# Performance work log

Measured on AMD Instinct MI355X. Metric: run time of the kernel, lower is better.

## Reference

```python
import jax, jax.numpy as jnp
import numpy as np

RNN = 1024     # rnn_size
POSE = 135     # config.pose_size (15 joints x 3x3 rotmat)
SEED = 120     # seed_seq_len
TGT = 24       # target_seq_len
B = 256        # batch size


def setup_inputs() -> dict:
    key = jax.random.key(0)
    k0, k1, k2, k3, k4 = jax.random.split(key, 5)
    s = 1.0 / np.sqrt(RNN)
    poses = jax.random.normal(k0, (B, SEED + TGT, POSE), dtype=jnp.float32)
    # nn.LSTMCell(input_size, rnn_size, bias=False): weights U(-1/sqrt(H), 1/sqrt(H))
    W_ih = jax.random.uniform(k1, (4 * RNN, POSE), minval=-s, maxval=s, dtype=jnp.float32)
    W_hh = jax.random.uniform(k2, (4 * RNN, RNN), minval=-s, maxval=s, dtype=jnp.float32)
    # nn.Linear(rnn_size, pose_size)
    W_fc = jax.random.uniform(k3, (POSE, RNN), minval=-s, maxval=s, dtype=jnp.float32)
    b_fc = jax.random.uniform(k4, (POSE,), minval=-s, maxval=s, dtype=jnp.float32)
    return {"poses": poses, "W_ih": W_ih, "W_hh": W_hh, "W_fc": W_fc, "b_fc": b_fc}


def reference(poses, W_ih, W_hh, W_fc, b_fc):
    def cell(x, h, c):
        # PyTorch LSTMCell gate order: i, f, g, o ; bias=False
        gates = x @ W_ih.T + h @ W_hh.T          # [B, 4*RNN]
        i, f, g, o = jnp.split(gates, 4, axis=-1)
        c_new = jax.nn.sigmoid(f) * c + jax.nn.sigmoid(i) * jnp.tanh(g)
        h_new = jax.nn.sigmoid(o) * jnp.tanh(c_new)
        return h_new, c_new

    # Encoder: steps over poses[:, 0:SEED-1] (dropout p=0 -> identity)
    enc_inputs = jnp.transpose(poses[:, : SEED - 1], (1, 0, 2))  # [SEED-1, B, POSE]
    h0 = jnp.zeros((B, RNN), dtype=poses.dtype)
    c0 = jnp.zeros((B, RNN), dtype=poses.dtype)

    def enc_step(carry, x):
        h, c = carry
        h, c = cell(x, h, c)
        return (h, c), None

    (h, c), _ = jax.lax.scan(enc_step, (h0, c0), enc_inputs)

    # first decoder input (poses[:, SEED-1]) is ground truth. inp is detached.
    inp0 = poses[:, SEED - 1]  # [B, POSE]

    def dec_step(carry, _):
        h, c, inp = carry
        inp = jax.lax.stop_gradient(inp)  # inp.detach() in the original
        h, c = cell(inp, h, c)
        out = inp + h @ W_fc.T + b_fc     # residual + linear decode
        return (h, c, out), out

    _, outs = jax.lax.scan(dec_step, (h, c, inp0), None, length=TGT)  # [TGT, B, POSE]
    return jnp.transpose(outs, (1, 0, 2))  # predictions [B, TGT, POSE]
```

## Files before the change

kernel.cpp:

```cpp
#include <hip/hip_runtime.h>
#include <stdint.h>

#define NB 256
#define NH 1024
#define NPOSE 135
#define NPPAD 160
#define NSTEPS 143
#define NDEC 24
#define KTOT 1184
#define LSTR 168
#define NWG 256

typedef __bf16 bf16;
typedef __attribute__((ext_vector_type(8))) __bf16 bf16x8;
typedef __attribute__((ext_vector_type(4))) float f32x4;
typedef __attribute__((ext_vector_type(4))) uint32_t u32x4;

#define WCAT_OFF 0
#define WCAT_BYTES (4096l * KTOT * 2)
#define WFC_OFF  (WCAT_OFF + WCAT_BYTES)
#define WFC_BYTES (144l * 1024 * 2)
#define X_OFF    (WFC_OFF + WFC_BYTES)
#define X_BYTES  (143l * NB * NPPAD * 2)
#define H_OFF    (X_OFF + X_BYTES)
#define H_BYTES  (2l * NB * NH * 2)
#define BAR_OFF  (H_OFF + H_BYTES)
#define BAR_BYTES 16384

__device__ __forceinline__ u32x4 llc_ld16(const void* p) {
  u32x4 v;
  asm volatile("global_load_dwordx4 %0, %1, off sc0 sc1"
               : "=v"(v) : "v"(p) : "memory");
  return v;
}
__device__ __forceinline__ u32x4 g_ld16(const void* p) {
  u32x4 v;
  asm volatile("global_load_dwordx4 %0, %1, off"
               : "=v"(v) : "v"(p) : "memory");
  return v;
}
__device__ __forceinline__ void llc_st2(void* p, uint32_t v) {
  asm volatile("global_store_short %0, %1, off sc0 sc1"
               :: "v"(p), "v"(v) : "memory");
}
#define WAIT_VM(n) do { \
    asm volatile("s_waitcnt vmcnt(" #n ")" ::: "memory"); \
    __builtin_amdgcn_sched_barrier(0); } while (0)

#define POLL(ptr, tgt) do { \
    while (__hip_atomic_load((ptr), __ATOMIC_RELAXED, __HIP_MEMORY_SCOPE_AGENT) < (tgt)) \
      __builtin_amdgcn_s_sleep(1); \
  } while (0)

__global__ void k_zero(uint32_t* p, int n) {
  int i = blockIdx.x * blockDim.x + threadIdx.x;
  int st = gridDim.x * blockDim.x;
  for (; i < n; i += st) p[i] = 0u;
}

__global__ void k_wcat(const float* __restrict__ Whh, const float* __restrict__ Wih,
                       bf16* __restrict__ W) {
  int n = blockIdx.x;
  for (int kk = threadIdx.x; kk < KTOT; kk += blockDim.x) {
    float v = 0.f;
    if (kk < NH) v = Whh[(size_t)n * NH + kk];
    else if (kk - NH < NPOSE) v = Wih[(size_t)n * NPOSE + (kk - NH)];
    W[(size_t)n * KTOT + kk] = (bf16)v;
  }
}

__global__ void k_wfc(const float* __restrict__ Wfc, bf16* __restrict__ W) {
  int p = blockIdx.x;
  for (int kk = threadIdx.x; kk < NH; kk += blockDim.x) {
    float v = (p < NPOSE) ? Wfc[(size_t)p * NH + kk] : 0.f;
    W[(size_t)p * NH + kk] = (bf16)v;
  }
}

__global__ void k_x(const float* __restrict__ poses, bf16* __restrict__ X) {
  int idx = blockIdx.x;
  int t = idx >> 8, b = idx & 255;
  int p = threadIdx.x;
  if (p < NPPAD) {
    float v = (p < NPOSE) ? poses[((size_t)b * 144 + t) * NPOSE + p] : 0.f;
    X[(size_t)idx * NPPAD + p] = (bf16)v;
  }
}

__device__ __forceinline__ float sigm(float x) { return 1.f / (1.f + __expf(-x)); }
__device__ __forceinline__ float tanh_(float x) {
  float e = __expf(2.f * x);
  return 1.f - 2.f / (e + 1.f);
}

__global__ __launch_bounds__(256, 1) void
k_main(const float* __restrict__ poses, const float* __restrict__ bfc,
       const bf16* __restrict__ Wcat, const bf16* __restrict__ Wfcb,
       bf16* __restrict__ X, bf16* __restrict__ H, int* __restrict__ bar,
       float* __restrict__ out) {
  __shared__ bf16 BldsH[8 * 64 * 128];
  __shared__ bf16 BldsX[64 * LSTR];

  const int tid  = threadIdx.x;
  const int lane = tid & 63;
  const int wv   = tid >> 6;
  const int cl   = lane & 15;
  const int quad = lane >> 4;
  const int L    = blockIdx.x;
  const int jb = (L & 7) * 8 + ((L >> 3) & 7);
  const int bb = L >> 6;
  const int b0 = bb * 64;
  const int j0 = jb * 16;
  const int mych = jb >> 3;
  const bool is_out = ((L & 7) == 7) && (((L >> 3) & 7) < 4);
  const int brow0 = bb * 64 + ((L >> 3) & 7) * 16;

  for (int t = tid; t < 8 * 64 * 16; t += 256) {
    int c = t >> 10, rem = t & 1023, r = rem >> 4, xb = rem & 15;
    u32x4 v = *(const u32x4*)&Wcat[(size_t)((r >> 4) * NH + j0 + (r & 15)) * KTOT
                                   + c * 128 + xb * 8];
    *(u32x4*)&BldsH[(c * 64 + r) * 128 + ((xb ^ (r & 15)) << 3)] = v;
  }
  for (int it = 0; it < 5; ++it) {
    int u = tid + it * 256, r = u / 20, iu = u % 20;
    u32x4 v = *(const u32x4*)&Wcat[(size_t)((r >> 4) * NH + j0 + (r & 15)) * KTOT
                                   + 1024 + iu * 8];
    *(u32x4*)&BldsX[r * LSTR + iu * 8] = v;
  }
  __syncthreads();

  const int arow = b0 + wv * 16 + cl;
  const size_t aBase  = (size_t)arow * NH + quad * 8;
  const size_t axBase = (size_t)arow * NPPAD + quad * 8;

  u32x4 A0[4], A1[4], A2[4], AX[5];
  f32x4 acc[4];
  float cst[4] = {0.f, 0.f, 0.f, 0.f};

#define ISSUE_AH(SET, HP, chn) do { \
    const bf16* ga_ = (HP) + aBase + (chn) * 128; \
    SET[0] = llc_ld16(ga_);      SET[1] = llc_ld16(ga_ + 32); \
    SET[2] = llc_ld16(ga_ + 64); SET[3] = llc_ld16(ga_ + 96); } while (0)
#define ISSUE_AX(sv) do { \
    const bf16* ga_ = X + (size_t)(sv) * NB * NPPAD + axBase; \
    if ((sv) < 120) { \
      AX[0] = g_ld16(ga_);        AX[1] = g_ld16(ga_ + 32); \
      AX[2] = g_ld16(ga_ + 64);   AX[3] = g_ld16(ga_ + 96); \
      AX[4] = g_ld16(ga_ + 128); \
    } else { \
      AX[0] = llc_ld16(ga_);      AX[1] = llc_ld16(ga_ + 32); \
      AX[2] = llc_ld16(ga_ + 64); AX[3] = llc_ld16(ga_ + 96); \
      AX[4] = llc_ld16(ga_ + 128); \
    } } while (0)
#define MFMA_LDS(SET, c) do { \
    _Pragma("unroll") \
    for (int ks = 0; ks < 4; ++ks) { \
      bf16x8 af_ = __builtin_bit_cast(bf16x8, SET[ks]); \
      _Pragma("unroll") \
      for (int gb = 0; gb < 4; ++gb) { \
        bf16x8 bw_ = *(const bf16x8*)&BldsH[((c) * 64 + gb * 16 + cl) * 128 \
                                            + (((ks * 4 + quad) ^ cl) << 3)]; \
        acc[gb] = __builtin_amdgcn_mfma_f32_16x16x32_bf16(af_, bw_, acc[gb], 0, 0, 0); \
      } } } while (0)
#define MFMA_X() do { \
    _Pragma("unroll") \
    for (int ks = 0; ks < 5; ++ks) { \
      bf16x8 af_ = __builtin_bit_cast(bf16x8, AX[ks]); \
      _Pragma("unroll") \
      for (int gb = 0; gb < 4; ++gb) { \
        bf16x8 bw_ = *(const bf16x8*)&BldsX[(gb * 16 + cl) * LSTR + ks * 32 + quad * 8]; \
        acc[gb] = __builtin_amdgcn_mfma_f32_16x16x32_bf16(af_, bw_, acc[gb], 0, 0, 0); \
      } } } while (0)
#define POLL_ALL8(tgt) do { \
    for (;;) { int ok_ = 1; \
      _Pragma("unroll") \
      for (int c_ = 0; c_ < 8; ++c_) \
        ok_ &= (__hip_atomic_load(&bar[(bb * 8 + c_) * 32], __ATOMIC_RELAXED, \
                                  __HIP_MEMORY_SCOPE_AGENT) >= (tgt)); \
      if (ok_) break; __builtin_amdgcn_s_sleep(1); } } while (0)

  ISSUE_AH(A0, H, 0);
  ISSUE_AH(A1, H, 1);

  for (int s = 0; s < NSTEPS; ++s) {
    const bf16* Hr = H + (size_t)(s & 1) * (NB * NH);
    bf16* Hw = H + (size_t)((s + 1) & 1) * (NB * NH);
    #pragma unroll
    for (int gb = 0; gb < 4; ++gb) acc[gb] = f32x4{0, 0, 0, 0};

    ISSUE_AH(A2, Hr, 2); WAIT_VM(8); MFMA_LDS(A0, 0);
    ISSUE_AH(A0, Hr, 3); WAIT_VM(8); MFMA_LDS(A1, 1);
    ISSUE_AH(A1, Hr, 4); WAIT_VM(8); MFMA_LDS(A2, 2);
    ISSUE_AH(A2, Hr, 5); WAIT_VM(8); MFMA_LDS(A0, 3);
    ISSUE_AH(A0, Hr, 6); WAIT_VM(8); MFMA_LDS(A1, 4);
    ISSUE_AH(A1, Hr, 7); WAIT_VM(8); MFMA_LDS(A2, 5);
    if (s >= 120) POLL(&bar[(32 + bb) * 32], 4 * (s - 119));
    ISSUE_AX(s);         WAIT_VM(9); MFMA_LDS(A0, 6);
                         WAIT_VM(5); MFMA_LDS(A1, 7);
                         WAIT_VM(0); MFMA_X();

    #pragma unroll
    for (int r = 0; r < 4; ++r) {
      float gi = sigm(acc[0][r]);
      float gf = sigm(acc[1][r]);
      float gg = tanh_(acc[2][r]);
      float go = sigm(acc[3][r]);
      float cn = gf * cst[r] + gi * gg;
      cst[r] = cn;
      float h = go * tanh_(cn);
      bf16 hb = (bf16)h;
      llc_st2(&Hw[(size_t)(b0 + wv * 16 + quad * 4 + r) * NH + j0 + cl],
              (uint32_t)__builtin_bit_cast(uint16_t, hb));
    }
    WAIT_VM(0);
    __syncthreads();
    if (tid == 0) atomicAdd(&bar[(bb * 8 + mych) * 32], 1);

    if (s >= 119 && is_out) {
      const int k = s - 119;
      POLL_ALL8(8 * (s + 1));
      f32x4 oa[3] = {{0,0,0,0},{0,0,0,0},{0,0,0,0}};
      const bf16* hrow = Hw + (size_t)(brow0 + cl) * NH;
      for (int kb = 0; kb < 4; ++kb) {
        u32x4 hv[8];
        #pragma unroll
        for (int t = 0; t < 8; ++t)
          hv[t] = llc_ld16(&hrow[(kb * 8 + t) * 32 + quad * 8]);
        WAIT_VM(0);
        #pragma unroll
        for (int t = 0; t < 8; ++t) {
          bf16x8 af = __builtin_bit_cast(bf16x8, hv[t]);
          #pragma unroll
          for (int i = 0; i < 3; ++i) {
            int ct = wv + i * 4;
            if (ct > 8) continue;
            bf16x8 bw = *(const bf16x8*)&Wfcb[(size_t)(ct * 16 + cl) * NH
                                              + (kb * 8 + t) * 32 + quad * 8];
            oa[i] = __builtin_amdgcn_mfma_f32_16x16x32_bf16(af, bw, oa[i], 0, 0, 0);
          }
        }
      }
      #pragma unroll
      for (int i = 0; i < 3; ++i) {
        int ct = wv + i * 4;
        if (ct > 8) continue;
        int p = ct * 16 + cl;
        if (p < NPOSE) {
          #pragma unroll
          for (int r = 0; r < 4; ++r) {
            int b = brow0 + quad * 4 + r;
            float inp = (k == 0) ? poses[((size_t)b * 144 + 119) * NPOSE + p]
                                 : out[((size_t)b * NDEC + (k - 1)) * NPOSE + p];
            float v = oa[i][r] + inp + bfc[p];
            out[((size_t)b * NDEC + k) * NPOSE + p] = v;
            if (s + 1 < NSTEPS) {
              bf16 xb = (bf16)v;
              llc_st2(&X[((size_t)(s + 1) * NB + b) * NPPAD + p],
                      (uint32_t)__builtin_bit_cast(uint16_t, xb));
            }
          }
        }
      }
      if (s + 1 < NSTEPS) {
        WAIT_VM(0);
        __syncthreads();
        if (tid == 0) atomicAdd(&bar[(32 + bb) * 32], 1);
      }
    }

    if (s + 1 < NSTEPS) {
      POLL_ALL8(8 * (s + 1));
      ISSUE_AH(A0, Hw, 0);
      ISSUE_AH(A1, Hw, 1);
    }
  }
}

extern "C" void kernel_launch(void* const* d_in, const int* in_sizes, int n_in,
                              void* d_out, int out_size, void* d_ws, size_t ws_size,
                              hipStream_t stream) {
  const float* poses = (const float*)d_in[0];
  const float* Wih   = (const float*)d_in[1];
  const float* Whh   = (const float*)d_in[2];
  const float* Wfc   = (const float*)d_in[3];
  const float* bfc   = (const float*)d_in[4];
  if (ws_size < (size_t)(BAR_OFF + BAR_BYTES)) return;

  char* ws = (char*)d_ws;
  bf16* Wcat = (bf16*)(ws + WCAT_OFF);
  bf16* Wfcb = (bf16*)(ws + WFC_OFF);
  bf16* X    = (bf16*)(ws + X_OFF);
  bf16* H    = (bf16*)(ws + H_OFF);
  int*  bar  = (int*)(ws + BAR_OFF);

  k_zero<<<256, 256, 0, stream>>>((uint32_t*)(ws + H_OFF), (int)((H_BYTES + BAR_BYTES) / 4));
  k_zero<<<256, 256, 0, stream>>>((uint32_t*)(X + (size_t)120 * NB * NPPAD),
                                  (int)(23l * NB * NPPAD * 2 / 4));
  k_wcat<<<4096, 256, 0, stream>>>(Whh, Wih, Wcat);
  k_wfc<<<144, 256, 0, stream>>>(Wfc, Wfcb);
  k_x<<<120 * 256, 256, 0, stream>>>(poses, X);
  k_main<<<NWG, 256, 0, stream>>>(poses, bfc, Wcat, Wfcb, X, H, bar, (float*)d_out);
}
```

Measured before the change: 1.644 ms.

## Switch recurrent GEMM to 32x32x16 MFMA with two-wave workgroups

Each workgroup now runs 2 waves instead of 4, each wave owning 32 batch rows and issuing 32x32x16 bf16 MFMAs into two 16-float accumulators. The four gates are regrouped with cross-lane shuffles before the cell update. Three H chunks are prefetched ahead instead of two, and the 8-counter barrier poll becomes one lane-parallel load reduced with __all. The aim is fewer MFMA and LDS read instructions per step and cheaper polling, at the cost of more registers per wave and fewer waves to hide latency.

```diff
diff --git a/kernel.cpp b/kernel.cpp
--- a/kernel.cpp
+++ b/kernel.cpp
@@ -14,6 +14,7 @@
 typedef __bf16 bf16;
 typedef __attribute__((ext_vector_type(8))) __bf16 bf16x8;
 typedef __attribute__((ext_vector_type(4))) float f32x4;
+typedef __attribute__((ext_vector_type(16))) float f32x16;
 typedef __attribute__((ext_vector_type(4))) uint32_t u32x4;
 
 #define WCAT_OFF 0
@@ -51,6 +52,13 @@
     while (__hip_atomic_load((ptr), __ATOMIC_RELAXED, __HIP_MEMORY_SCOPE_AGENT) < (tgt)) \
       __builtin_amdgcn_s_sleep(1); \
   } while (0)
+#define POLL_ALL8(tgt) do { \
+    for (;;) { \
+      int v_ = __hip_atomic_load(&bar[(bb * 8 + (lane & 7)) * 32], \
+                                 __ATOMIC_RELAXED, __HIP_MEMORY_SCOPE_AGENT); \
+      if (__all(v_ >= (tgt))) break; \
+      __builtin_amdgcn_s_sleep(1); \
+    } } while (0)
 
 __global__ void k_zero(uint32_t* p, int n) {
   int i = blockIdx.x * blockDim.x + threadIdx.x;
@@ -93,7 +101,7 @@
   return 1.f - 2.f / (e + 1.f);
 }
 
-__global__ __launch_bounds__(256, 1) void
+__global__ __launch_bounds__(128, 1) void
 k_main(const float* __restrict__ poses, const float* __restrict__ bfc,
        const bf16* __restrict__ Wcat, const bf16* __restrict__ Wfcb,
        bf16* __restrict__ X, bf16* __restrict__ H, int* __restrict__ bar,
@@ -104,6 +112,9 @@
   const int tid  = threadIdx.x;
   const int lane = tid & 63;
   const int wv   = tid >> 6;
+  const int lrow = lane & 31;
+  const int half = lane >> 5;
+  const int l15  = lane & 15;
   const int cl   = lane & 15;
   const int quad = lane >> 4;
   const int L    = blockIdx.x;
@@ -115,101 +126,102 @@
   const bool is_out = ((L & 7) == 7) && (((L >> 3) & 7) < 4);
   const int brow0 = bb * 64 + ((L >> 3) & 7) * 16;
 
-  for (int t = tid; t < 8 * 64 * 16; t += 256) {
+  for (int t = tid; t < 8 * 64 * 16; t += 128) {
     int c = t >> 10, rem = t & 1023, r = rem >> 4, xb = rem & 15;
     u32x4 v = *(const u32x4*)&Wcat[(size_t)((r >> 4) * NH + j0 + (r & 15)) * KTOT
                                    + c * 128 + xb * 8];
     *(u32x4*)&BldsH[(c * 64 + r) * 128 + ((xb ^ (r & 15)) << 3)] = v;
   }
-  for (int it = 0; it < 5; ++it) {
-    int u = tid + it * 256, r = u / 20, iu = u % 20;
+  for (int t = tid; t < 64 * 20; t += 128) {
+    int r = t / 20, iu = t % 20;
     u32x4 v = *(const u32x4*)&Wcat[(size_t)((r >> 4) * NH + j0 + (r & 15)) * KTOT
                                    + 1024 + iu * 8];
     *(u32x4*)&BldsX[r * LSTR + iu * 8] = v;
   }
   __syncthreads();
 
-  const int arow = b0 + wv * 16 + cl;
-  const size_t aBase  = (size_t)arow * NH + quad * 8;
-  const size_t axBase = (size_t)arow * NPPAD + quad * 8;
-
-  u32x4 A0[4], A1[4], A2[4], AX[5];
-  f32x4 acc[4];
-  float cst[4] = {0.f, 0.f, 0.f, 0.f};
+  const int arow = b0 + 32 * wv + lrow;
+  const size_t aBase  = (size_t)arow * NH + half * 8;
+  const size_t axBase = (size_t)arow * NPPAD + half * 8;
+
+  u32x4 A0[8], A1[8], A2[8], AX[10];
+  f32x16 acc0, acc1;
+  float cst[8];
+  #pragma unroll
+  for (int r = 0; r < 8; ++r) cst[r] = 0.f;
 
 #define ISSUE_AH(SET, HP, chn) do { \
     const bf16* ga_ = (HP) + aBase + (chn) * 128; \
-    SET[0] = llc_ld16(ga_);      SET[1] = llc_ld16(ga_ + 32); \
-    SET[2] = llc_ld16(ga_ + 64); SET[3] = llc_ld16(ga_ + 96); } while (0)
+    _Pragma("unroll") \
+    for (int kk_ = 0; kk_ < 8; ++kk_) SET[kk_] = llc_ld16(ga_ + kk_ * 16); } while (0)
 #define ISSUE_AX(sv) do { \
     const bf16* ga_ = X + (size_t)(sv) * NB * NPPAD + axBase; \
     if ((sv) < 120) { \
-      AX[0] = g_ld16(ga_);        AX[1] = g_ld16(ga_ + 32); \
-      AX[2] = g_ld16(ga_ + 64);   AX[3] = g_ld16(ga_ + 96); \
-      AX[4] = g_ld16(ga_ + 128); \
+      _Pragma("unroll") \
+      for (int kk_ = 0; kk_ < 10; ++kk_) AX[kk_] = g_ld16(ga_ + kk_ * 16); \
     } else { \
-      AX[0] = llc_ld16(ga_);      AX[1] = llc_ld16(ga_ + 32); \
-      AX[2] = llc_ld16(ga_ + 64); AX[3] = llc_ld16(ga_ + 96); \
-      AX[4] = llc_ld16(ga_ + 128); \
+      _Pragma("unroll") \
+      for (int kk_ = 0; kk_ < 10; ++kk_) AX[kk_] = llc_ld16(ga_ + kk_ * 16); \
     } } while (0)
-#define MFMA_LDS(SET, c) do { \
+#define MFMA_H(SET, c) do { \
     _Pragma("unroll") \
-    for (int ks = 0; ks < 4; ++ks) { \
-      bf16x8 af_ = __builtin_bit_cast(bf16x8, SET[ks]); \
-      _Pragma("unroll") \
-      for (int gb = 0; gb < 4; ++gb) { \
-        bf16x8 bw_ = *(const bf16x8*)&BldsH[((c) * 64 + gb * 16 + cl) * 128 \
-                                            + (((ks * 4 + quad) ^ cl) << 3)]; \
-        acc[gb] = __builtin_amdgcn_mfma_f32_16x16x32_bf16(af_, bw_, acc[gb], 0, 0, 0); \
-      } } } while (0)
+    for (int kk_ = 0; kk_ < 8; ++kk_) { \
+      bf16x8 af_ = __builtin_bit_cast(bf16x8, SET[kk_]); \
+      int slot_ = ((kk_ * 2 + half) ^ l15) << 3; \
+      bf16x8 b0_ = *(const bf16x8*)&BldsH[((c) * 64 + lrow) * 128 + slot_]; \
+      bf16x8 b1_ = *(const bf16x8*)&BldsH[((c) * 64 + 32 + lrow) * 128 + slot_]; \
+      acc0 = __builtin_amdgcn_mfma_f32_32x32x16_bf16(af_, b0_, acc0, 0, 0, 0); \
+      acc1 = __builtin_amdgcn_mfma_f32_32x32x16_bf16(af_, b1_, acc1, 0, 0, 0); \
+    } } while (0)
 #define MFMA_X() do { \
     _Pragma("unroll") \
-    for (int ks = 0; ks < 5; ++ks) { \
-      bf16x8 af_ = __builtin_bit_cast(bf16x8, AX[ks]); \
-      _Pragma("unroll") \
-      for (int gb = 0; gb < 4; ++gb) { \
-        bf16x8 bw_ = *(const bf16x8*)&BldsX[(gb * 16 + cl) * LSTR + ks * 32 + quad * 8]; \
-        acc[gb] = __builtin_amdgcn_mfma_f32_16x16x32_bf16(af_, bw_, acc[gb], 0, 0, 0); \
-      } } } while (0)
-#define POLL_ALL8(tgt) do { \
-    for (;;) { int ok_ = 1; \
-      _Pragma("unroll") \
-      for (int c_ = 0; c_ < 8; ++c_) \
-        ok_ &= (__hip_atomic_load(&bar[(bb * 8 + c_) * 32], __ATOMIC_RELAXED, \
-                                  __HIP_MEMORY_SCOPE_AGENT) >= (tgt)); \
-      if (ok_) break; __builtin_amdgcn_s_sleep(1); } } while (0)
+    for (int kk_ = 0; kk_ < 10; ++kk_) { \
+      bf16x8 af_ = __builtin_bit_cast(bf16x8, AX[kk_]); \
+      bf16x8 b0_ = *(const bf16x8*)&BldsX[lrow * LSTR + kk_ * 16 + half * 8]; \
+      bf16x8 b1_ = *(const bf16x8*)&BldsX[(32 + lrow) * LSTR + kk_ * 16 + half * 8]; \
+      acc0 = __builtin_amdgcn_mfma_f32_32x32x16_bf16(af_, b0_, acc0, 0, 0, 0); \
+      acc1 = __builtin_amdgcn_mfma_f32_32x32x16_bf16(af_, b1_, acc1, 0, 0, 0); \
+    } } while (0)
 
   ISSUE_AH(A0, H, 0);
   ISSUE_AH(A1, H, 1);
+  ISSUE_AH(A2, H, 2);
 
   for (int s = 0; s < NSTEPS; ++s) {
     const bf16* Hr = H + (size_t)(s & 1) * (NB * NH);
     bf16* Hw = H + (size_t)((s + 1) & 1) * (NB * NH);
+    acc0 = (f32x16)(0.f); acc1 = (f32x16)(0.f);
+
+    WAIT_VM(16); MFMA_H(A0, 0); ISSUE_AH(A0, Hr, 3);
+    WAIT_VM(16); MFMA_H(A1, 1); ISSUE_AH(A1, Hr, 4);
+    WAIT_VM(16); MFMA_H(A2, 2); ISSUE_AH(A2, Hr, 5);
+    WAIT_VM(16); MFMA_H(A0, 3); ISSUE_AH(A0, Hr, 6);
+    WAIT_VM(16); MFMA_H(A1, 4); ISSUE_AH(A1, Hr, 7);
+    WAIT_VM(16); MFMA_H(A2, 5);
+    if (s >= 120) POLL(&bar[(32 + bb) * 32], 4 * (s - 119));
+    ISSUE_AX(s);
+    WAIT_VM(18); MFMA_H(A0, 6);
+    WAIT_VM(10); MFMA_H(A1, 7);
+    WAIT_VM(0);  MFMA_X();
+
     #pragma unroll
-    for (int gb = 0; gb < 4; ++gb) acc[gb] = f32x4{0, 0, 0, 0};
-
-    ISSUE_AH(A2, Hr, 2); WAIT_VM(8); MFMA_LDS(A0, 0);
-    ISSUE_AH(A0, Hr, 3); WAIT_VM(8); MFMA_LDS(A1, 1);
-    ISSUE_AH(A1, Hr, 4); WAIT_VM(8); MFMA_LDS(A2, 2);
-    ISSUE_AH(A2, Hr, 5); WAIT_VM(8); MFMA_LDS(A0, 3);
-    ISSUE_AH(A0, Hr, 6); WAIT_VM(8); MFMA_LDS(A1, 4);
-    ISSUE_AH(A1, Hr, 7); WAIT_VM(8); MFMA_LDS(A2, 5);
-    if (s >= 120) POLL(&bar[(32 + bb) * 32], 4 * (s - 119));
-    ISSUE_AX(s);         WAIT_VM(9); MFMA_LDS(A0, 6);
-                         WAIT_VM(5); MFMA_LDS(A1, 7);
-                         WAIT_VM(0); MFMA_X();
-
-    #pragma unroll
-    for (int r = 0; r < 4; ++r) {
-      float gi = sigm(acc[0][r]);
-      float gf = sigm(acc[1][r]);
-      float gg = tanh_(acc[2][r]);
-      float go = sigm(acc[3][r]);
-      float cn = gf * cst[r] + gi * gg;
-      cst[r] = cn;
-      float h = go * tanh_(cn);
+    for (int r8 = 0; r8 < 8; ++r8) {
+      float s0a = __shfl_xor(acc0[r8], 16);
+      float s0b = __shfl_xor(acc0[r8 + 8], 16);
+      float s1a = __shfl_xor(acc1[r8], 16);
+      float s1b = __shfl_xor(acc1[r8 + 8], 16);
+      const bool lo = (lrow < 16);
+      float iv = lo ? acc0[r8]     : s0b;
+      float fv = lo ? s0a          : acc0[r8 + 8];
+      float gv = lo ? acc1[r8]     : s1b;
+      float ov = lo ? s1a          : acc1[r8 + 8];
+      int reg  = lo ? r8 : (r8 + 8);
+      float cn = sigm(fv) * cst[r8] + sigm(iv) * tanh_(gv);
+      cst[r8] = cn;
+      float h = sigm(ov) * tanh_(cn);
+      int row32 = (reg & 3) + 8 * (reg >> 2) + 4 * half;
       bf16 hb = (bf16)h;
-      llc_st2(&Hw[(size_t)(b0 + wv * 16 + quad * 4 + r) * NH + j0 + cl],
+      llc_st2(&Hw[(size_t)(b0 + 32 * wv + row32) * NH + j0 + l15],
               (uint32_t)__builtin_bit_cast(uint16_t, hb));
     }
     WAIT_VM(0);
@@ -219,7 +231,7 @@
     if (s >= 119 && is_out) {
       const int k = s - 119;
       POLL_ALL8(8 * (s + 1));
-      f32x4 oa[3] = {{0,0,0,0},{0,0,0,0},{0,0,0,0}};
+      f32x4 oa[5] = {{0,0,0,0},{0,0,0,0},{0,0,0,0},{0,0,0,0},{0,0,0,0}};
       const bf16* hrow = Hw + (size_t)(brow0 + cl) * NH;
       for (int kb = 0; kb < 4; ++kb) {
         u32x4 hv[8];
@@ -231,8 +243,8 @@
         for (int t = 0; t < 8; ++t) {
           bf16x8 af = __builtin_bit_cast(bf16x8, hv[t]);
           #pragma unroll
-          for (int i = 0; i < 3; ++i) {
-            int ct = wv + i * 4;
+          for (int i = 0; i < 5; ++i) {
+            int ct = wv + i * 2;
             if (ct > 8) continue;
             bf16x8 bw = *(const bf16x8*)&Wfcb[(size_t)(ct * 16 + cl) * NH
                                               + (kb * 8 + t) * 32 + quad * 8];
@@ -241,8 +253,8 @@
         }
       }
       #pragma unroll
-      for (int i = 0; i < 3; ++i) {
-        int ct = wv + i * 4;
+      for (int i = 0; i < 5; ++i) {
+        int ct = wv + i * 2;
         if (ct > 8) continue;
         int p = ct * 16 + cl;
         if (p < NPOSE) {
@@ -272,6 +284,7 @@
       POLL_ALL8(8 * (s + 1));
       ISSUE_AH(A0, Hw, 0);
       ISSUE_AH(A1, Hw, 1);
+      ISSUE_AH(A2, Hw, 2);
     }
   }
 }
@@ -299,5 +312,5 @@
   k_wcat<<<4096, 256, 0, stream>>>(Whh, Wih, Wcat);
   k_wfc<<<144, 256, 0, stream>>>(Wfc, Wfcb);
   k_x<<<120 * 256, 256, 0, stream>>>(poses, X);
-  k_main<<<NWG, 256, 0, stream>>>(poses, bfc, Wcat, Wfcb, X, H, bar, (float*)d_out);
-}
+  k_main<<<NWG, 128, 0, stream>>>(poses, bfc, Wcat, Wfcb, X, H, bar, (float*)d_out);
+}
```

New measurement: 2.426 ms. +47.6%, slower.

## Give every LSTM step its own hidden-state buffer so reads can use cached loads

Applied to the files above, without the earlier changes.

When the workspace is large enough, the hidden state gets a separate buffer per timestep (144 slices) instead of a double buffer. Each address is then written only once, so H and the decoder-step X reads can switch from cache-bypassing sc0/sc1 loads to ordinary cached loads without the risk of reading stale data. The barrier poll across the eight column groups also becomes one load per lane with a wave-wide vote instead of eight sequential loads. The cost is a much larger workspace footprint, and correctness now depends on no stale lines existing for freshly written addresses.

```diff
diff --git a/kernel.cpp b/kernel.cpp
--- a/kernel.cpp
+++ b/kernel.cpp
@@ -23,8 +23,8 @@
 #define X_OFF    (WFC_OFF + WFC_BYTES)
 #define X_BYTES  (143l * NB * NPPAD * 2)
 #define H_OFF    (X_OFF + X_BYTES)
-#define H_BYTES  (2l * NB * NH * 2)
-#define BAR_OFF  (H_OFF + H_BYTES)
+#define H_BYTES2    (2l * NB * NH * 2)
+#define H_BYTES144  (144l * NB * NH * 2)
 #define BAR_BYTES 16384
 
 __device__ __forceinline__ u32x4 llc_ld16(const void* p) {
@@ -39,6 +39,9 @@
                : "=v"(v) : "v"(p) : "memory");
   return v;
 }
+__device__ __forceinline__ u32x4 ld16sel(const void* p, bool cached) {
+  return cached ? g_ld16(p) : llc_ld16(p);
+}
 __device__ __forceinline__ void llc_st2(void* p, uint32_t v) {
   asm volatile("global_store_short %0, %1, off sc0 sc1"
                :: "v"(p), "v"(v) : "memory");
@@ -51,6 +54,13 @@
     while (__hip_atomic_load((ptr), __ATOMIC_RELAXED, __HIP_MEMORY_SCOPE_AGENT) < (tgt)) \
       __builtin_amdgcn_s_sleep(1); \
   } while (0)
+#define POLL_ALL8(tgt) do { \
+    for (;;) { \
+      int v_ = __hip_atomic_load(&bar[(bb * 8 + (lane & 7)) * 32], \
+                                 __ATOMIC_RELAXED, __HIP_MEMORY_SCOPE_AGENT); \
+      if (__all(v_ >= (tgt))) break; \
+      __builtin_amdgcn_s_sleep(1); \
+    } } while (0)
 
 __global__ void k_zero(uint32_t* p, int n) {
   int i = blockIdx.x * blockDim.x + threadIdx.x;
@@ -93,6 +103,7 @@
   return 1.f - 2.f / (e + 1.f);
 }
 
+template <bool DEEP>
 __global__ __launch_bounds__(256, 1) void
 k_main(const float* __restrict__ poses, const float* __restrict__ bfc,
        const bf16* __restrict__ Wcat, const bf16* __restrict__ Wfcb,
@@ -139,8 +150,8 @@
 
 #define ISSUE_AH(SET, HP, chn) do { \
     const bf16* ga_ = (HP) + aBase + (chn) * 128; \
-    SET[0] = llc_ld16(ga_);      SET[1] = llc_ld16(ga_ + 32); \
-    SET[2] = llc_ld16(ga_ + 64); SET[3] = llc_ld16(ga_ + 96); } while (0)
+    SET[0] = ld16sel(ga_, DEEP);      SET[1] = ld16sel(ga_ + 32, DEEP); \
+    SET[2] = ld16sel(ga_ + 64, DEEP); SET[3] = ld16sel(ga_ + 96, DEEP); } while (0)
 #define ISSUE_AX(sv) do { \
     const bf16* ga_ = X + (size_t)(sv) * NB * NPPAD + axBase; \
     if ((sv) < 120) { \
@@ -148,9 +159,9 @@
       AX[2] = g_ld16(ga_ + 64);   AX[3] = g_ld16(ga_ + 96); \
       AX[4] = g_ld16(ga_ + 128); \
     } else { \
-      AX[0] = llc_ld16(ga_);      AX[1] = llc_ld16(ga_ + 32); \
-      AX[2] = llc_ld16(ga_ + 64); AX[3] = llc_ld16(ga_ + 96); \
-      AX[4] = llc_ld16(ga_ + 128); \
+      AX[0] = ld16sel(ga_, DEEP);       AX[1] = ld16sel(ga_ + 32, DEEP); \
+      AX[2] = ld16sel(ga_ + 64, DEEP);  AX[3] = ld16sel(ga_ + 96, DEEP); \
+      AX[4] = ld16sel(ga_ + 128, DEEP); \
     } } while (0)
 #define MFMA_LDS(SET, c) do { \
     _Pragma("unroll") \
@@ -171,20 +182,13 @@
         bf16x8 bw_ = *(const bf16x8*)&BldsX[(gb * 16 + cl) * LSTR + ks * 32 + quad * 8]; \
         acc[gb] = __builtin_amdgcn_mfma_f32_16x16x32_bf16(af_, bw_, acc[gb], 0, 0, 0); \
       } } } while (0)
-#define POLL_ALL8(tgt) do { \
-    for (;;) { int ok_ = 1; \
-      _Pragma("unroll") \
-      for (int c_ = 0; c_ < 8; ++c_) \
-        ok_ &= (__hip_atomic_load(&bar[(bb * 8 + c_) * 32], __ATOMIC_RELAXED, \
-                                  __HIP_MEMORY_SCOPE_AGENT) >= (tgt)); \
-      if (ok_) break; __builtin_amdgcn_s_sleep(1); } } while (0)
 
   ISSUE_AH(A0, H, 0);
   ISSUE_AH(A1, H, 1);
 
   for (int s = 0; s < NSTEPS; ++s) {
-    const bf16* Hr = H + (size_t)(s & 1) * (NB * NH);
-    bf16* Hw = H + (size_t)((s + 1) & 1) * (NB * NH);
+    const bf16* Hr = H + (size_t)(DEEP ? s : (s & 1)) * (NB * NH);
+    bf16* Hw = H + (size_t)(DEEP ? (s + 1) : ((s + 1) & 1)) * (NB * NH);
     #pragma unroll
     for (int gb = 0; gb < 4; ++gb) acc[gb] = f32x4{0, 0, 0, 0};
 
@@ -225,7 +229,7 @@
         u32x4 hv[8];
         #pragma unroll
         for (int t = 0; t < 8; ++t)
-          hv[t] = llc_ld16(&hrow[(kb * 8 + t) * 32 + quad * 8]);
+          hv[t] = ld16sel(&hrow[(kb * 8 + t) * 32 + quad * 8], DEEP);
         WAIT_VM(0);
         #pragma unroll
         for (int t = 0; t < 8; ++t) {
@@ -284,20 +288,36 @@
   const float* Whh   = (const float*)d_in[2];
   const float* Wfc   = (const float*)d_in[3];
   const float* bfc   = (const float*)d_in[4];
-  if (ws_size < (size_t)(BAR_OFF + BAR_BYTES)) return;
+
+  const size_t need_deep = (size_t)H_OFF + H_BYTES144 + BAR_BYTES;
+  const size_t need_min  = (size_t)H_OFF + H_BYTES2 + BAR_BYTES;
+  if (ws_size < need_min) return;
+  const bool deep = ws_size >= need_deep;
+  const size_t hbytes = deep ? (size_t)H_BYTES144 : (size_t)H_BYTES2;
 
   char* ws = (char*)d_ws;
   bf16* Wcat = (bf16*)(ws + WCAT_OFF);
   bf16* Wfcb = (bf16*)(ws + WFC_OFF);
   bf16* X    = (bf16*)(ws + X_OFF);
   bf16* H    = (bf16*)(ws + H_OFF);
-  int*  bar  = (int*)(ws + BAR_OFF);
-
-  k_zero<<<256, 256, 0, stream>>>((uint32_t*)(ws + H_OFF), (int)((H_BYTES + BAR_BYTES) / 4));
+  int*  bar  = (int*)(ws + H_OFF + hbytes);
+
+  if (deep) {
+    k_zero<<<256, 256, 0, stream>>>((uint32_t*)(ws + H_OFF), (int)(NB * NH * 2 / 4));
+    k_zero<<<32, 256, 0, stream>>>((uint32_t*)bar, BAR_BYTES / 4);
+  } else {
+    k_zero<<<256, 256, 0, stream>>>((uint32_t*)(ws + H_OFF),
+                                    (int)((H_BYTES2 + BAR_BYTES) / 4));
+  }
   k_zero<<<256, 256, 0, stream>>>((uint32_t*)(X + (size_t)120 * NB * NPPAD),
                                   (int)(23l * NB * NPPAD * 2 / 4));
   k_wcat<<<4096, 256, 0, stream>>>(Whh, Wih, Wcat);
   k_wfc<<<144, 256, 0, stream>>>(Wfc, Wfcb);
   k_x<<<120 * 256, 256, 0, stream>>>(poses, X);
-  k_main<<<NWG, 256, 0, stream>>>(poses, bfc, Wcat, Wfcb, X, H, bar, (float*)d_out);
-}
+  if (deep)
+    k_main<true><<<NWG, 256, 0, stream>>>(poses, bfc, Wcat, Wfcb, X, H, bar,
+                                          (float*)d_out);
+  else
+    k_main<false><<<NWG, 256, 0, stream>>>(poses, bfc, Wcat, Wfcb, X, H, bar,
+                                           (float*)d_out);
+}
```

Measured after the change: 1.610 ms. -2.0%, faster.
